# Kernel optimization log

Measured on AMD Instinct MI355X. Metric: run time of the kernel, lower is better.

Reference implementation:

```python
import jax, jax.numpy as jnp
import numpy as np

B, N, P, F = 4, 131072, 512, 32  # batch, points per batch, plane_size, feature_dim


def setup_inputs() -> dict:
    key = jax.random.key(0)
    k1, k2 = jax.random.split(key)
    coords = jax.random.uniform(k1, (B, N, 3), jnp.float32, -1.0, 1.0)
    # torch.nn.init.uniform_(tplanes, -0.01, 0.01)
    tplanes = jax.random.uniform(k2, (3, P, P, F), jnp.float32, -0.01, 0.01)
    return {"coords": coords, "tplanes": tplanes}


def _bilerp(plane, uv):
    # plane: [P, P, F] laid out [H(v), W(u), C]; uv: [M, 2] in [0, 1]
    # matches nvdiffrast texture(filter_mode='linear', boundary_mode='clamp',
    # max_mip_level=0): texel centers at (i + 0.5) / P, clamp-to-edge.
    Ps = plane.shape[0]
    x = jnp.clip(uv[:, 0] * Ps - 0.5, 0.0, Ps - 1.0)
    y = jnp.clip(uv[:, 1] * Ps - 0.5, 0.0, Ps - 1.0)
    x0f = jnp.floor(x)
    y0f = jnp.floor(y)
    xi0 = x0f.astype(jnp.int32)
    yi0 = y0f.astype(jnp.int32)
    xi1 = jnp.minimum(xi0 + 1, Ps - 1)
    yi1 = jnp.minimum(yi0 + 1, Ps - 1)
    fx = (x - x0f)[:, None]  # [M, 1]
    fy = (y - y0f)[:, None]
    f00 = plane[yi0, xi0]  # [M, F]
    f01 = plane[yi0, xi1]
    f10 = plane[yi1, xi0]
    f11 = plane[yi1, xi1]
    return (f00 * (1.0 - fx) + f01 * fx) * (1.0 - fy) + (f10 * (1.0 - fx) + f11 * fx) * fy


def reference(coords, tplanes):
    batch_size = coords.shape[0]
    c = coords * 0.5 + 0.5          # [-1,1] -> [0,1]
    c = c.reshape(-1, 3)            # [M, 3]
    # plane 0 samples (x, y); plane 1 samples (x, z); plane 2 samples (z, y)
    uvs = jnp.stack([c[:, (0, 1)], c[:, (0, 2)], c[:, (2, 1)]], axis=0)  # [3, M, 2]
    feats = jax.vmap(_bilerp)(tplanes, uvs)        # [3, M, F]
    feats = jnp.transpose(feats, (1, 0, 2))        # [M, 3, F]
    out = feats.reshape(batch_size, -1, 3 * F)     # concat over planes: [B, N, 3F]
    return out
```

## Files before the change

kernel.cpp:

```cpp
#include <hip/hip_runtime.h>


#define PS 512
#define FDIM 32

__global__ __launch_bounds__(256) void tplanes_enc_kernel(
    const float* __restrict__ coords,
    const float* __restrict__ tplanes,
    float* __restrict__ out,
    int M)
{
    int tid = blockIdx.x * blockDim.x + threadIdx.x;
    int total = M * 3 * (FDIM / 4);
    if (tid >= total) return;

    int chunk = tid & 7;
    int pp    = tid >> 3;
    int plane = pp % 3;
    int point = pp / 3;

    float cx = coords[point * 3 + 0] * 0.5f + 0.5f;
    float cy = coords[point * 3 + 1] * 0.5f + 0.5f;
    float cz = coords[point * 3 + 2] * 0.5f + 0.5f;

    float u = (plane == 2) ? cz : cx;
    float v = (plane == 1) ? cz : cy;

    float x = fminf(fmaxf(u * (float)PS - 0.5f, 0.0f), (float)(PS - 1));
    float y = fminf(fmaxf(v * (float)PS - 0.5f, 0.0f), (float)(PS - 1));
    float x0f = floorf(x);
    float y0f = floorf(y);
    int xi0 = (int)x0f;
    int yi0 = (int)y0f;
    int xi1 = min(xi0 + 1, PS - 1);
    int yi1 = min(yi0 + 1, PS - 1);
    float fx = x - x0f;
    float fy = y - y0f;

    const float4* base = (const float4*)(tplanes + (size_t)plane * PS * PS * FDIM);
    int o00 = (yi0 * PS + xi0) * 8 + chunk;
    int o01 = (yi0 * PS + xi1) * 8 + chunk;
    int o10 = (yi1 * PS + xi0) * 8 + chunk;
    int o11 = (yi1 * PS + xi1) * 8 + chunk;

    float4 f00 = base[o00];
    float4 f01 = base[o01];
    float4 f10 = base[o10];
    float4 f11 = base[o11];

    float gx = 1.0f - fx;
    float gy = 1.0f - fy;
    float4 r;
    r.x = (f00.x * gx + f01.x * fx) * gy + (f10.x * gx + f11.x * fx) * fy;
    r.y = (f00.y * gx + f01.y * fx) * gy + (f10.y * gx + f11.y * fx) * fy;
    r.z = (f00.z * gx + f01.z * fx) * gy + (f10.z * gx + f11.z * fx) * fy;
    r.w = (f00.w * gx + f01.w * fx) * gy + (f10.w * gx + f11.w * fx) * fy;

    ((float4*)out)[(size_t)pp * 8 + chunk] = r;
}

extern "C" void kernel_launch(void* const* d_in, const int* in_sizes, int n_in,
                              void* d_out, int out_size, void* d_ws, size_t ws_size,
                              hipStream_t stream) {
    const float* coords  = (const float*)d_in[0];
    const float* tplanes = (const float*)d_in[1];
    float* out = (float*)d_out;

    int M = in_sizes[0] / 3;
    int total = M * 3 * (FDIM / 4);
    int block = 256;
    int grid = (total + block - 1) / block;
    tplanes_enc_kernel<<<grid, block, 0, stream>>>(coords, tplanes, out, M);
}
```

Measured before the change: 355.2 us.

## Process two output chunks per thread and use nontemporal output stores

Each thread now handles two work items, one from the first half and one from the second half of the index space. It computes all addresses first, then issues all eight gather loads before any arithmetic, which raises memory-level parallelism. Output is written with nontemporal stores so the large output stream does not evict plane data from cache. The cost is more registers per thread and half as many threads, and the two items a thread handles are far apart in memory.

```diff
diff --git a/kernel.cpp b/kernel.cpp
--- a/kernel.cpp
+++ b/kernel.cpp
@@ -4,59 +4,84 @@
 #define PS 512
 #define FDIM 32
 
+typedef float floatx4 __attribute__((ext_vector_type(4)));
+
 __global__ __launch_bounds__(256) void tplanes_enc_kernel(
     const float* __restrict__ coords,
     const float* __restrict__ tplanes,
     float* __restrict__ out,
-    int M)
+    int M, int total, int half)
 {
     int tid = blockIdx.x * blockDim.x + threadIdx.x;
-    int total = M * 3 * (FDIM / 4);
-    if (tid >= total) return;
 
-    int chunk = tid & 7;
-    int pp    = tid >> 3;
-    int plane = pp % 3;
-    int point = pp / 3;
+    int  idxs[2];
+    bool valid[2];
+    idxs[0] = tid;
+    idxs[1] = tid + half;
+    valid[0] = idxs[0] < total;
+    valid[1] = idxs[1] < total;
 
-    float cx = coords[point * 3 + 0] * 0.5f + 0.5f;
-    float cy = coords[point * 3 + 1] * 0.5f + 0.5f;
-    float cz = coords[point * 3 + 2] * 0.5f + 0.5f;
+    const floatx4* base[2];
+    int o00[2], o01[2], o10[2], o11[2];
+    float fx[2], fy[2];
 
-    float u = (plane == 2) ? cz : cx;
-    float v = (plane == 1) ? cz : cy;
+#pragma unroll
+    for (int k = 0; k < 2; ++k) {
+        if (!valid[k]) continue;
+        int idx   = idxs[k];
+        int chunk = idx & 7;
+        int pp    = idx >> 3;
+        int plane = pp % 3;
+        int point = pp / 3;
 
-    float x = fminf(fmaxf(u * (float)PS - 0.5f, 0.0f), (float)(PS - 1));
-    float y = fminf(fmaxf(v * (float)PS - 0.5f, 0.0f), (float)(PS - 1));
-    float x0f = floorf(x);
-    float y0f = floorf(y);
-    int xi0 = (int)x0f;
-    int yi0 = (int)y0f;
-    int xi1 = min(xi0 + 1, PS - 1);
-    int yi1 = min(yi0 + 1, PS - 1);
-    float fx = x - x0f;
-    float fy = y - y0f;
+        float cx = coords[point * 3 + 0] * 0.5f + 0.5f;
+        float cy = coords[point * 3 + 1] * 0.5f + 0.5f;
+        float cz = coords[point * 3 + 2] * 0.5f + 0.5f;
 
-    const float4* base = (const float4*)(tplanes + (size_t)plane * PS * PS * FDIM);
-    int o00 = (yi0 * PS + xi0) * 8 + chunk;
-    int o01 = (yi0 * PS + xi1) * 8 + chunk;
-    int o10 = (yi1 * PS + xi0) * 8 + chunk;
-    int o11 = (yi1 * PS + xi1) * 8 + chunk;
+        float u = (plane == 2) ? cz : cx;
+        float v = (plane == 1) ? cz : cy;
 
-    float4 f00 = base[o00];
-    float4 f01 = base[o01];
-    float4 f10 = base[o10];
-    float4 f11 = base[o11];
+        float x = fminf(fmaxf(u * (float)PS - 0.5f, 0.0f), (float)(PS - 1));
+        float y = fminf(fmaxf(v * (float)PS - 0.5f, 0.0f), (float)(PS - 1));
+        float x0f = floorf(x);
+        float y0f = floorf(y);
+        int xi0 = (int)x0f;
+        int yi0 = (int)y0f;
+        int xi1 = min(xi0 + 1, PS - 1);
+        int yi1 = min(yi0 + 1, PS - 1);
+        fx[k] = x - x0f;
+        fy[k] = y - y0f;
 
-    float gx = 1.0f - fx;
-    float gy = 1.0f - fy;
-    float4 r;
-    r.x = (f00.x * gx + f01.x * fx) * gy + (f10.x * gx + f11.x * fx) * fy;
-    r.y = (f00.y * gx + f01.y * fx) * gy + (f10.y * gx + f11.y * fx) * fy;
-    r.z = (f00.z * gx + f01.z * fx) * gy + (f10.z * gx + f11.z * fx) * fy;
-    r.w = (f00.w * gx + f01.w * fx) * gy + (f10.w * gx + f11.w * fx) * fy;
+        base[k] = (const floatx4*)(tplanes + (size_t)plane * PS * PS * FDIM);
+        o00[k] = (yi0 * PS + xi0) * 8 + chunk;
+        o01[k] = (yi0 * PS + xi1) * 8 + chunk;
+        o10[k] = (yi1 * PS + xi0) * 8 + chunk;
+        o11[k] = (yi1 * PS + xi1) * 8 + chunk;
+    }
 
-    ((float4*)out)[(size_t)pp * 8 + chunk] = r;
+    floatx4 f00[2], f01[2], f10[2], f11[2];
+#pragma unroll
+    for (int k = 0; k < 2; ++k) {
+        if (!valid[k]) continue;
+        f00[k] = base[k][o00[k]];
+        f01[k] = base[k][o01[k]];
+        f10[k] = base[k][o10[k]];
+        f11[k] = base[k][o11[k]];
+    }
+
+#pragma unroll
+    for (int k = 0; k < 2; ++k) {
+        if (!valid[k]) continue;
+        float fxk = fx[k], fyk = fy[k];
+        float gx = 1.0f - fxk;
+        float gy = 1.0f - fyk;
+        floatx4 r;
+        r.x = (f00[k].x * gx + f01[k].x * fxk) * gy + (f10[k].x * gx + f11[k].x * fxk) * fyk;
+        r.y = (f00[k].y * gx + f01[k].y * fxk) * gy + (f10[k].y * gx + f11[k].y * fxk) * fyk;
+        r.z = (f00[k].z * gx + f01[k].z * fxk) * gy + (f10[k].z * gx + f11[k].z * fxk) * fyk;
+        r.w = (f00[k].w * gx + f01[k].w * fxk) * gy + (f10[k].w * gx + f11[k].w * fxk) * fyk;
+        __builtin_nontemporal_store(r, (floatx4*)out + idxs[k]);
+    }
 }
 
 extern "C" void kernel_launch(void* const* d_in, const int* in_sizes, int n_in,
@@ -68,7 +93,8 @@
 
     int M = in_sizes[0] / 3;
     int total = M * 3 * (FDIM / 4);
+    int half  = (total + 1) / 2;
     int block = 256;
-    int grid = (total + block - 1) / block;
-    tplanes_enc_kernel<<<grid, block, 0, stream>>>(coords, tplanes, out, M);
+    int grid = (half + block - 1) / block;
+    tplanes_enc_kernel<<<grid, block, 0, stream>>>(coords, tplanes, out, M, total, half);
 }
```

New measurement: 352.2 us. No clear change (-0.8%).

## Use persistent grid-stride kernel with software-pipelined gathers and nontemporal stores

Applied to the files above, without the earlier changes.

Replaces the one-thread-per-chunk launch with a fixed 2048-block grid-stride loop. Each thread processes two items per iteration and computes the next pair's coordinates and offsets while the current gathers are in flight. Output is written with nontemporal stores so it does not evict texture plane data from cache. This adds register pressure and fixes the grid size, which may hurt occupancy or load balance.

```diff
diff --git a/kernel.cpp b/kernel.cpp
--- a/kernel.cpp
+++ b/kernel.cpp
@@ -4,18 +4,27 @@
 #define PS 512
 #define FDIM 32
 
-__global__ __launch_bounds__(256) void tplanes_enc_kernel(
-    const float* __restrict__ coords,
-    const float* __restrict__ tplanes,
-    float* __restrict__ out,
-    int M)
+typedef float floatx4 __attribute__((ext_vector_type(4)));
+
+struct Item {
+    const floatx4* base;
+    int o00, o01, o10, o11;
+    float fx, fy;
+    int oidx;
+    bool valid;
+};
+
+__device__ __forceinline__ Item prep(int idx, int total,
+                                     const float* __restrict__ coords,
+                                     const float* __restrict__ tplanes)
 {
-    int tid = blockIdx.x * blockDim.x + threadIdx.x;
-    int total = M * 3 * (FDIM / 4);
-    if (tid >= total) return;
+    Item it;
+    it.valid = (idx < total);
+    it.oidx  = idx;
+    int safe = it.valid ? idx : 0;
 
-    int chunk = tid & 7;
-    int pp    = tid >> 3;
+    int chunk = safe & 7;
+    int pp    = safe >> 3;
     int plane = pp % 3;
     int point = pp / 3;
 
@@ -34,29 +43,66 @@
     int yi0 = (int)y0f;
     int xi1 = min(xi0 + 1, PS - 1);
     int yi1 = min(yi0 + 1, PS - 1);
-    float fx = x - x0f;
-    float fy = y - y0f;
+    it.fx = x - x0f;
+    it.fy = y - y0f;
 
-    const float4* base = (const float4*)(tplanes + (size_t)plane * PS * PS * FDIM);
-    int o00 = (yi0 * PS + xi0) * 8 + chunk;
-    int o01 = (yi0 * PS + xi1) * 8 + chunk;
-    int o10 = (yi1 * PS + xi0) * 8 + chunk;
-    int o11 = (yi1 * PS + xi1) * 8 + chunk;
+    it.base = (const floatx4*)(tplanes + (size_t)plane * PS * PS * FDIM);
+    it.o00 = (yi0 * PS + xi0) * 8 + chunk;
+    it.o01 = (yi0 * PS + xi1) * 8 + chunk;
+    it.o10 = (yi1 * PS + xi0) * 8 + chunk;
+    it.o11 = (yi1 * PS + xi1) * 8 + chunk;
+    return it;
+}
 
-    float4 f00 = base[o00];
-    float4 f01 = base[o01];
-    float4 f10 = base[o10];
-    float4 f11 = base[o11];
-
+__device__ __forceinline__ void finish(const Item& it,
+                                       floatx4 f00, floatx4 f01,
+                                       floatx4 f10, floatx4 f11,
+                                       float* __restrict__ out)
+{
+    if (!it.valid) return;
+    float fx = it.fx, fy = it.fy;
     float gx = 1.0f - fx;
     float gy = 1.0f - fy;
-    float4 r;
+    floatx4 r;
     r.x = (f00.x * gx + f01.x * fx) * gy + (f10.x * gx + f11.x * fx) * fy;
     r.y = (f00.y * gx + f01.y * fx) * gy + (f10.y * gx + f11.y * fx) * fy;
     r.z = (f00.z * gx + f01.z * fx) * gy + (f10.z * gx + f11.z * fx) * fy;
     r.w = (f00.w * gx + f01.w * fx) * gy + (f10.w * gx + f11.w * fx) * fy;
+    __builtin_nontemporal_store(r, (floatx4*)out + it.oidx);
+}
 
-    ((float4*)out)[(size_t)pp * 8 + chunk] = r;
+__global__ __launch_bounds__(256) void tplanes_enc_kernel(
+    const float* __restrict__ coords,
+    const float* __restrict__ tplanes,
+    float* __restrict__ out,
+    int total, int stride)
+{
+    int tid = blockIdx.x * blockDim.x + threadIdx.x;
+
+    Item a = prep(tid,          total, coords, tplanes);
+    Item b = prep(tid + stride, total, coords, tplanes);
+
+    for (int i = tid; i < total; ) {
+        floatx4 a00{}, a01{}, a10{}, a11{};
+        floatx4 b00{}, b01{}, b10{}, b11{};
+        if (a.valid) {
+            a00 = a.base[a.o00]; a01 = a.base[a.o01];
+            a10 = a.base[a.o10]; a11 = a.base[a.o11];
+        }
+        if (b.valid) {
+            b00 = b.base[b.o00]; b01 = b.base[b.o01];
+            b10 = b.base[b.o10]; b11 = b.base[b.o11];
+        }
+
+        int ni = i + 2 * stride;
+        Item na = prep(ni,          total, coords, tplanes);
+        Item nb = prep(ni + stride, total, coords, tplanes);
+
+        finish(a, a00, a01, a10, a11, out);
+        finish(b, b00, b01, b10, b11, out);
+
+        a = na; b = nb; i = ni;
+    }
 }
 
 extern "C" void kernel_launch(void* const* d_in, const int* in_sizes, int n_in,
@@ -69,6 +115,7 @@
     int M = in_sizes[0] / 3;
     int total = M * 3 * (FDIM / 4);
     int block = 256;
-    int grid = (total + block - 1) / block;
-    tplanes_enc_kernel<<<grid, block, 0, stream>>>(coords, tplanes, out, M);
+    int grid  = 2048;
+    int stride = grid * block;
+    tplanes_enc_kernel<<<grid, block, 0, stream>>>(coords, tplanes, out, total, stride);
 }
```

After: 354.2 us. About the same (-0.3%).

## Convert triplane features to fp16 in workspace and gather half-precision texels

Applied to the files above, without the earlier changes.

Adds a pre-pass that converts the fp32 triplanes into an fp16 copy in the workspace, then runs a sampling kernel that gathers 8 halfs per load, with four threads per point-plane instead of eight. Output stores become nontemporal. The aim is to halve gather traffic and cache footprint for the random bilinear lookups, at the cost of an extra conversion pass over about 100MB of planes on every call and reduced precision in the features. Falls back to the fp32 kernel when the workspace is too small.

```diff
diff --git a/kernel.cpp b/kernel.cpp
--- a/kernel.cpp
+++ b/kernel.cpp
@@ -4,18 +4,37 @@
 #define PS 512
 #define FDIM 32
 
-__global__ __launch_bounds__(256) void tplanes_enc_kernel(
+typedef float    floatx4 __attribute__((ext_vector_type(4)));
+typedef _Float16 halfx8  __attribute__((ext_vector_type(8)));
+
+__global__ __launch_bounds__(256) void convert_kernel(
+    const floatx4* __restrict__ in,
+    halfx8* __restrict__ out8,
+    int n8)
+{
+    int t = blockIdx.x * blockDim.x + threadIdx.x;
+    if (t >= n8) return;
+    floatx4 a = in[2 * t];
+    floatx4 b = in[2 * t + 1];
+    halfx8 h;
+    h[0] = (_Float16)a.x; h[1] = (_Float16)a.y;
+    h[2] = (_Float16)a.z; h[3] = (_Float16)a.w;
+    h[4] = (_Float16)b.x; h[5] = (_Float16)b.y;
+    h[6] = (_Float16)b.z; h[7] = (_Float16)b.w;
+    out8[t] = h;
+}
+
+__global__ __launch_bounds__(256) void tplanes_enc_fp16_kernel(
     const float* __restrict__ coords,
-    const float* __restrict__ tplanes,
+    const _Float16* __restrict__ tp16,
     float* __restrict__ out,
-    int M)
+    int total)
 {
     int tid = blockIdx.x * blockDim.x + threadIdx.x;
-    int total = M * 3 * (FDIM / 4);
     if (tid >= total) return;
 
-    int chunk = tid & 7;
-    int pp    = tid >> 3;
+    int chunk = tid & 3;
+    int pp    = tid >> 2;
     int plane = pp % 3;
     int point = pp / 3;
 
@@ -37,26 +56,87 @@
     float fx = x - x0f;
     float fy = y - y0f;
 
-    const float4* base = (const float4*)(tplanes + (size_t)plane * PS * PS * FDIM);
+    const halfx8* base = (const halfx8*)tp16 + (size_t)plane * PS * PS * (FDIM / 8);
+    int o00 = (yi0 * PS + xi0) * 4 + chunk;
+    int o01 = (yi0 * PS + xi1) * 4 + chunk;
+    int o10 = (yi1 * PS + xi0) * 4 + chunk;
+    int o11 = (yi1 * PS + xi1) * 4 + chunk;
+
+    halfx8 f00 = base[o00];
+    halfx8 f01 = base[o01];
+    halfx8 f10 = base[o10];
+    halfx8 f11 = base[o11];
+
+    float gx = 1.0f - fx;
+    float gy = 1.0f - fy;
+
+    floatx4 r0, r1;
+#pragma unroll
+    for (int j = 0; j < 4; ++j) {
+        r0[j] = ((float)f00[j] * gx + (float)f01[j] * fx) * gy
+              + ((float)f10[j] * gx + (float)f11[j] * fx) * fy;
+    }
+#pragma unroll
+    for (int j = 0; j < 4; ++j) {
+        r1[j] = ((float)f00[j + 4] * gx + (float)f01[j + 4] * fx) * gy
+              + ((float)f10[j + 4] * gx + (float)f11[j + 4] * fx) * fy;
+    }
+
+    int ob = pp * 8 + chunk * 2;
+    __builtin_nontemporal_store(r0, (floatx4*)out + ob);
+    __builtin_nontemporal_store(r1, (floatx4*)out + ob + 1);
+}
+
+__global__ __launch_bounds__(256) void tplanes_enc_f32_kernel(
+    const float* __restrict__ coords,
+    const float* __restrict__ tplanes,
+    float* __restrict__ out,
+    int total)
+{
+    int tid = blockIdx.x * blockDim.x + threadIdx.x;
+    if (tid >= total) return;
+
+    int chunk = tid & 7;
+    int pp    = tid >> 3;
+    int plane = pp % 3;
+    int point = pp / 3;
+
+    float cx = coords[point * 3 + 0] * 0.5f + 0.5f;
+    float cy = coords[point * 3 + 1] * 0.5f + 0.5f;
+    float cz = coords[point * 3 + 2] * 0.5f + 0.5f;
+    float u = (plane == 2) ? cz : cx;
+    float v = (plane == 1) ? cz : cy;
+
+    float x = fminf(fmaxf(u * (float)PS - 0.5f, 0.0f), (float)(PS - 1));
+    float y = fminf(fmaxf(v * (float)PS - 0.5f, 0.0f), (float)(PS - 1));
+    float x0f = floorf(x);
+    float y0f = floorf(y);
+    int xi0 = (int)x0f;
+    int yi0 = (int)y0f;
+    int xi1 = min(xi0 + 1, PS - 1);
+    int yi1 = min(yi0 + 1, PS - 1);
+    float fx = x - x0f;
+    float fy = y - y0f;
+
+    const floatx4* base = (const floatx4*)(tplanes + (size_t)plane * PS * PS * FDIM);
     int o00 = (yi0 * PS + xi0) * 8 + chunk;
     int o01 = (yi0 * PS + xi1) * 8 + chunk;
     int o10 = (yi1 * PS + xi0) * 8 + chunk;
     int o11 = (yi1 * PS + xi1) * 8 + chunk;
 
-    float4 f00 = base[o00];
-    float4 f01 = base[o01];
-    float4 f10 = base[o10];
-    float4 f11 = base[o11];
+    floatx4 f00 = base[o00];
+    floatx4 f01 = base[o01];
+    floatx4 f10 = base[o10];
+    floatx4 f11 = base[o11];
 
     float gx = 1.0f - fx;
     float gy = 1.0f - fy;
-    float4 r;
+    floatx4 r;
     r.x = (f00.x * gx + f01.x * fx) * gy + (f10.x * gx + f11.x * fx) * fy;
     r.y = (f00.y * gx + f01.y * fx) * gy + (f10.y * gx + f11.y * fx) * fy;
     r.z = (f00.z * gx + f01.z * fx) * gy + (f10.z * gx + f11.z * fx) * fy;
     r.w = (f00.w * gx + f01.w * fx) * gy + (f10.w * gx + f11.w * fx) * fy;
-
-    ((float4*)out)[(size_t)pp * 8 + chunk] = r;
+    __builtin_nontemporal_store(r, (floatx4*)out + (size_t)pp * 8 + chunk);
 }
 
 extern "C" void kernel_launch(void* const* d_in, const int* in_sizes, int n_in,
@@ -67,8 +147,23 @@
     float* out = (float*)d_out;
 
     int M = in_sizes[0] / 3;
-    int total = M * 3 * (FDIM / 4);
+    const size_t planesN = (size_t)3 * PS * PS * FDIM;
+    const size_t need    = planesN * sizeof(_Float16);
+
     int block = 256;
-    int grid = (total + block - 1) / block;
-    tplanes_enc_kernel<<<grid, block, 0, stream>>>(coords, tplanes, out, M);
+    if (ws_size >= need) {
+        int n8 = (int)(planesN / 8);
+        int g1 = (n8 + block - 1) / block;
+        convert_kernel<<<g1, block, 0, stream>>>(
+            (const floatx4*)tplanes, (halfx8*)d_ws, n8);
+
+        int total = M * 3 * 4;
+        int g2 = (total + block - 1) / block;
+        tplanes_enc_fp16_kernel<<<g2, block, 0, stream>>>(
+            coords, (const _Float16*)d_ws, out, total);
+    } else {
+        int total = M * 3 * 8;
+        int g = (total + block - 1) / block;
+        tplanes_enc_f32_kernel<<<g, block, 0, stream>>>(coords, tplanes, out, total);
+    }
 }
```

Result: no change. 361.8 us (+1.9%).
